# Kernel tuning notes

Measured on AMD Instinct MI355X. Metric: run time of the kernel, lower is better.

Reference implementation:

```python
import jax, jax.numpy as jnp
import numpy as np
from jax.ops import segment_sum

N_NODES = 50000
N_EDGES = 800000
IN_DIM, HID_DIM, OUT_DIM = 128, 128, 64
N_GRAPHS = 64


def setup_inputs() -> dict:
    key = jax.random.key(0)
    ks = jax.random.split(key, 8)
    x = jax.random.normal(ks[0], (N_NODES, IN_DIM), dtype=jnp.float32)
    edge_index = jax.random.randint(ks[1], (2, N_EDGES), 0, N_NODES, dtype=jnp.int64)
    batch = jnp.sort(jax.random.randint(ks[2], (N_NODES,), 0, N_GRAPHS, dtype=jnp.int64))
    # Glorot-ish init for GCNConv linear weights, zero bias (PyG default)
    W1 = jax.random.normal(ks[3], (IN_DIM, HID_DIM), dtype=jnp.float32) / np.sqrt(IN_DIM)
    b1 = jnp.zeros((HID_DIM,), dtype=jnp.float32)
    W2 = jax.random.normal(ks[4], (HID_DIM, OUT_DIM), dtype=jnp.float32) / np.sqrt(HID_DIM)
    b2 = jnp.zeros((OUT_DIM,), dtype=jnp.float32)
    return {"x": x, "W1": W1, "b1": b1, "W2": W2, "b2": b2,
            "edge_index": edge_index, "batch": batch, "num_graphs": N_GRAPHS}


def _gcn_conv(h, W, b, src, dst, deg_inv_sqrt, n_nodes):
    # h: [N, Fin] -> [N, Fout]; GCNConv: D^{-1/2}(A+I)D^{-1/2} (h W) + b
    hw = h @ W                                   # [N, Fout]
    norm = deg_inv_sqrt[src] * deg_inv_sqrt[dst] # [E]
    msg = hw[src] * norm[:, None]                # [E, Fout] (gather)
    agg = segment_sum(msg, dst, num_segments=n_nodes)  # scatter-add
    # self-loop contribution: norm_ii = deg_inv_sqrt[i]^2
    agg = agg + hw * (deg_inv_sqrt * deg_inv_sqrt)[:, None]
    return agg + b


def reference(x, W1, b1, W2, b2, edge_index, batch, num_graphs):
    n_nodes = x.shape[0]
    src, dst = edge_index[0], edge_index[1]
    # degree of A + I (self-loops added, as in PyG GCNConv default)
    deg = segment_sum(jnp.ones_like(dst, dtype=x.dtype), dst,
                      num_segments=n_nodes) + 1.0
    deg_inv_sqrt = jax.lax.rsqrt(deg)

    h = jax.nn.relu(_gcn_conv(x, W1, b1, src, dst, deg_inv_sqrt, n_nodes))
    h = jax.nn.relu(_gcn_conv(h, W2, b2, src, dst, deg_inv_sqrt, n_nodes))

    # global_mean_pool over batch ids
    sums = segment_sum(h, batch, num_segments=num_graphs)          # [G, Fout]
    counts = segment_sum(jnp.ones((n_nodes,), dtype=h.dtype), batch,
                         num_segments=num_graphs)                  # [G]
    return sums / jnp.maximum(counts, 1.0)[:, None]
```

## Files before the change

### kernel.cpp

```cpp
#include <hip/hip_runtime.h>

typedef float f4 __attribute__((ext_vector_type(4)));
typedef float f2 __attribute__((ext_vector_type(2)));
typedef short s8 __attribute__((ext_vector_type(8)));

union FU { unsigned u[4]; s8 s; };

__device__ __forceinline__ unsigned cvtpk(float lo, float hi){
  unsigned r;
  asm("v_cvt_pk_bf16_f32 %0, %1, %2" : "=v"(r) : "v"(lo), "v"(hi));
  return r;
}

__device__ __forceinline__ float bflo(unsigned v){ return __uint_as_float(v << 16); }
__device__ __forceinline__ float bfhi(unsigned v){ return __uint_as_float(v & 0xFFFF0000u); }

__device__ __forceinline__ int ld_idx(const void* p, int i, int is64){
  if (is64) return (int)((const long long*)p)[i];
  return ((const int*)p)[i];
}

__device__ __forceinline__ int detect64(const unsigned* __restrict__ e_raw, int e){
  int lane = threadIdx.x & 63;
  int lim = (e < 1024) ? e : 1024;
  int nz = 0;
  for (int i = lane; i < lim; i += 64) nz |= (e_raw[2*i + 1] != 0u);
  return (__ballot(nz != 0) == 0ull) ? 1 : 0;
}

template<int NC>
__device__ __forceinline__ void gemm_body(const float* __restrict__ X,
                                          const float* __restrict__ W,
                                          unsigned short* __restrict__ Yb,
                                          int n, int blk, char* Alds){
  constexpr int NCF = NC/16;
  constexpr int WPC = 8/NCF;
  constexpr int RT  = 8/WPC;
  const int tid  = threadIdx.x;
  const int wave = tid >> 6, lane = tid & 63;
  const int rb = blk * 128;
  const f4* X4 = (const f4*)X;

  const int cbase = (wave % NCF) * 16;
  const int rt0   = (wave / NCF) * RT;
  const int col   = cbase + (lane & 15);
  const int kr0   = (lane >> 4) * 8;
  FU bu[4];
#pragma unroll
  for (int ks = 0; ks < 4; ++ks){
    float wv[8];
#pragma unroll
    for (int j = 0; j < 8; ++j) wv[j] = W[(size_t)(ks*32 + kr0 + j)*NC + col];
#pragma unroll
    for (int q = 0; q < 4; ++q) bu[ks].u[q] = cvtpk(wv[2*q], wv[2*q+1]);
  }

  for (int i = tid; i < 128*32; i += 512){
    int row = i >> 5, kq = i & 31;
    int rsrc = rb + row; if (rsrc >= n) rsrc = n - 1;
    f4 xv = X4[(size_t)rsrc*32 + kq];
    unsigned lo = cvtpk(xv[0], xv[1]), hi = cvtpk(xv[2], xv[3]);
    int byte = (row*256 + kq*8) ^ ((row & 7) << 4);
    *reinterpret_cast<uint2*>(Alds + byte) = make_uint2(lo, hi);
  }
  __syncthreads();

  f4 acc[RT];
#pragma unroll
  for (int rt = 0; rt < RT; ++rt) acc[rt] = 0.0f;

#pragma unroll
  for (int rt = 0; rt < RT; ++rt){
    const int arow = (rt0 + rt)*16 + (lane & 15);
#pragma unroll
    for (int ks = 0; ks < 4; ++ks){
      int kb = ks*32 + kr0;
      int byte = (arow*256 + kb*2) ^ ((arow & 7) << 4);
      s8 a = *reinterpret_cast<const s8*>(Alds + byte);
      acc[rt] = __builtin_amdgcn_mfma_f32_16x16x32_bf16(a, bu[ks].s, acc[rt], 0, 0, 0);
    }
  }

#pragma unroll
  for (int rt = 0; rt < RT; ++rt){
    int rowb = rb + (rt0 + rt)*16 + 4*(lane >> 4);
#pragma unroll
    for (int r = 0; r < 4; ++r){
      int row = rowb + r;
      if (row < n) Yb[(size_t)row*NC + col] = (unsigned short)cvtpk(acc[rt][r], acc[rt][r]);
    }
  }
}

template<int NC>
__global__ __launch_bounds__(512) void gemm_k(const float* __restrict__ X,
                                              const float* __restrict__ W,
                                              unsigned short* __restrict__ Yb, int n){
  __shared__ int4 AldsV[2048];
  gemm_body<NC>(X, W, Yb, n, blockIdx.x, (char*)AldsV);
}

__global__ __launch_bounds__(512) void fused1_k(const float* __restrict__ X,
                                                const float* __restrict__ W1,
                                                unsigned short* __restrict__ Yb,
                                                const void* __restrict__ eidx,
                                                const void* __restrict__ batchp,
                                                int* __restrict__ counts,
                                                int* __restrict__ batch32,
                                                int n, int e, int GB, int CB){
  __shared__ int4 AldsV[2048];
  __shared__ int hist[512];
  int blk = blockIdx.x;
  if (blk < GB){
    gemm_body<128>(X, W1, Yb, n, blk, (char*)AldsV);
    return;
  }
  blk -= GB;
  const int NBK = (n + 127) >> 7;
  for (int i = threadIdx.x; i < NBK; i += 512) hist[i] = 0;
  __syncthreads();
  int is64 = detect64((const unsigned*)eidx, e);
  int CHK = (e + CB - 1) / CB;
  int beg = blk*CHK, end = min(e, beg + CHK);
  for (int i = beg + (int)threadIdx.x; i < end; i += 512){
    int d = ld_idx(eidx, e + i, is64);
    atomicAdd(&hist[d >> 7], 1);
  }
  __syncthreads();
  for (int i = threadIdx.x; i < NBK; i += 512) counts[i*CB + blk] = hist[i];
  for (int i = blk*512 + (int)threadIdx.x; i < n; i += CB*512)
    batch32[i] = ld_idx(batchp, i, is64);
}

__global__ void scanA_k(const int* __restrict__ counts, int* __restrict__ base,
                        int* __restrict__ bsum, int L){
  __shared__ int sh[256];
  int tid = threadIdx.x;
  int i = blockIdx.x*256 + tid;
  int v = (i < L) ? counts[i] : 0;
  sh[tid] = v; __syncthreads();
  for (int off = 1; off < 256; off <<= 1){
    int t = (tid >= off) ? sh[tid - off] : 0;
    __syncthreads();
    sh[tid] += t;
    __syncthreads();
  }
  if (i < L) base[i] = sh[tid] - v;
  if (tid == 255) bsum[blockIdx.x] = sh[255];
}

__global__ __launch_bounds__(512) void scanB2_k(int* __restrict__ bsum, int nb,
                                                float* __restrict__ outsum,
                                                int totalOut){
  __shared__ int sh[512];
  int tid = threadIdx.x;
  int v = (tid < nb) ? bsum[tid] : 0;
  sh[tid] = v; __syncthreads();
  for (int off = 1; off < 512; off <<= 1){
    int t = (tid >= off) ? sh[tid - off] : 0;
    __syncthreads();
    sh[tid] += t;
    __syncthreads();
  }
  if (tid < nb) bsum[tid] = sh[tid] - v;
  for (int k = tid; k < totalOut; k += 512) outsum[k] = 0.0f;
}

__global__ void scanC_k(int* __restrict__ base, const int* __restrict__ bsum,
                        int* __restrict__ bb, int* __restrict__ rowptr,
                        int L, int CB, int NBK, int n, int e){
  int i = blockIdx.x*256 + threadIdx.x;
  if (i < L){
    int vfin = base[i] + bsum[i >> 8];
    base[i] = vfin;
    if ((i & (CB - 1)) == 0) bb[i / CB] = vfin;
  }
  if (i == 0){ bb[NBK] = e; rowptr[n] = e; }
}

__global__ __launch_bounds__(512) void scat_k(const void* __restrict__ eidx,
                                              const int* __restrict__ base,
                                              int* __restrict__ packed,
                                              int n, int e, int CB){
  __shared__ int cur[512];
  int blk = blockIdx.x, tid = threadIdx.x;
  const int NBK = (n + 127) >> 7;
  for (int i = tid; i < NBK; i += 512) cur[i] = base[i*CB + blk];
  __syncthreads();
  int is64 = detect64((const unsigned*)eidx, e);
  int CHK = (e + CB - 1) / CB;
  int beg = blk*CHK, end = min(e, beg + CHK);
  for (int i = beg + tid; i < end; i += 512){
    int s = ld_idx(eidx, i, is64);
    int d = ld_idx(eidx, e + i, is64);
    int pos = atomicAdd(&cur[d >> 7], 1);
    packed[pos] = s | ((d & 127) << 16);
  }
}

#define CSR_CAP 6144
__global__ __launch_bounds__(256) void csr_k(const int* __restrict__ packed,
                                             const int* __restrict__ bb,
                                             int* __restrict__ esrcS,
                                             int* __restrict__ rowptr,
                                             float* __restrict__ dinv, int n){
  __shared__ int vals[CSR_CAP];
  __shared__ int hist[128], off[128], cur[128];
  int b = blockIdx.x, tid = threadIdx.x;
  int sbeg = bb[b], send = bb[b + 1];
  int m = send - sbeg;
  int mL = min(m, CSR_CAP);
  for (int i = tid; i < mL; i += 256) vals[i] = packed[sbeg + i];
  if (tid < 128) hist[tid] = 0;
  __syncthreads();
  for (int i = tid; i < m; i += 256){
    int v = (i < CSR_CAP) ? vals[i] : packed[sbeg + i];
    atomicAdd(&hist[(v >> 16) & 127], 1);
  }
  __syncthreads();
  if (tid < 128) off[tid] = hist[tid];
  __syncthreads();
  for (int o = 1; o < 128; o <<= 1){
    int v = 0;
    if (tid < 128 && tid >= o) v = off[tid - o];
    __syncthreads();
    if (tid < 128) off[tid] += v;
    __syncthreads();
  }
  if (tid < 128){
    int ex = off[tid] - hist[tid];
    cur[tid] = ex;
    int node = b*128 + tid;
    if (node < n){
      rowptr[node] = sbeg + ex;
      dinv[node] = rsqrtf((float)hist[tid] + 1.0f);
    }
  }
  __syncthreads();
  for (int i = tid; i < m; i += 256){
    int v = (i < CSR_CAP) ? vals[i] : packed[sbeg + i];
    int pos = atomicAdd(&cur[(v >> 16) & 127], 1);
    esrcS[sbeg + pos] = v & 0xFFFF;
  }
}

template<int NC>
__global__ __launch_bounds__(256) void agg_k(const unsigned short* __restrict__ HWb,
                                             const float* __restrict__ dinv,
                                             const int* __restrict__ rowptr,
                                             const int* __restrict__ esrcS,
                                             const float* __restrict__ bias,
                                             float* __restrict__ Hout, int n){
  int wid  = (blockIdx.x*256 + threadIdx.x) >> 6;
  int lane = threadIdx.x & 63;
  if (wid >= n) return;
  wid = __builtin_amdgcn_readfirstlane(wid);
  float di = dinv[wid];
  float di2 = di * di;
  int beg = __builtin_amdgcn_readfirstlane(rowptr[wid]);
  int end = __builtin_amdgcn_readfirstlane(rowptr[wid + 1]);
  if (NC == 128){
    unsigned sv = ((const unsigned*)(HWb + (size_t)wid*128))[lane];
    f2 acc;
    acc[0] = bflo(sv) * di2;
    acc[1] = bfhi(sv) * di2;
    int j = beg;
    for (; j + 8 <= end; j += 8){
      int s[8]; float dv[8]; unsigned v[8];
#pragma unroll
      for (int t = 0; t < 8; ++t) s[t] = esrcS[j + t];
#pragma unroll
      for (int t = 0; t < 8; ++t){
        dv[t] = dinv[s[t]];
        v[t] = ((const unsigned*)(HWb + (size_t)s[t]*128))[lane];
      }
#pragma unroll
      for (int t = 0; t < 8; ++t){
        float wt = dv[t] * di;
        acc[0] += bflo(v[t]) * wt;
        acc[1] += bfhi(v[t]) * wt;
      }
    }
    if (j + 4 <= end){
      int s[4]; float dv[4]; unsigned v[4];
#pragma unroll
      for (int t = 0; t < 4; ++t) s[t] = esrcS[j + t];
#pragma unroll
      for (int t = 0; t < 4; ++t){
        dv[t] = dinv[s[t]];
        v[t] = ((const unsigned*)(HWb + (size_t)s[t]*128))[lane];
      }
#pragma unroll
      for (int t = 0; t < 4; ++t){
        float wt = dv[t] * di;
        acc[0] += bflo(v[t]) * wt;
        acc[1] += bfhi(v[t]) * wt;
      }
      j += 4;
    }
    for (; j < end; ++j){
      int s = esrcS[j];
      float wt = dinv[s] * di;
      unsigned v = ((const unsigned*)(HWb + (size_t)s*128))[lane];
      acc[0] += bflo(v) * wt;
      acc[1] += bfhi(v) * wt;
    }
    f2 bb2 = ((const f2*)bias)[lane];
    acc += bb2;
    acc[0] = fmaxf(acc[0], 0.0f);
    acc[1] = fmaxf(acc[1], 0.0f);
    ((f2*)Hout)[(size_t)wid*64 + lane] = acc;
  } else {
    float acc = bflo((unsigned)HWb[(size_t)wid*64 + lane]) * di2;
    int j = beg;
    for (; j + 8 <= end; j += 8){
      int s[8]; float dv[8]; unsigned v[8];
#pragma unroll
      for (int t = 0; t < 8; ++t) s[t] = esrcS[j + t];
#pragma unroll
      for (int t = 0; t < 8; ++t){
        dv[t] = dinv[s[t]];
        v[t] = (unsigned)HWb[(size_t)s[t]*64 + lane];
      }
#pragma unroll
      for (int t = 0; t < 8; ++t) acc += bflo(v[t]) * (dv[t] * di);
    }
    if (j + 4 <= end){
      int s[4]; float dv[4]; unsigned v[4];
#pragma unroll
      for (int t = 0; t < 4; ++t) s[t] = esrcS[j + t];
#pragma unroll
      for (int t = 0; t < 4; ++t){
        dv[t] = dinv[s[t]];
        v[t] = (unsigned)HWb[(size_t)s[t]*64 + lane];
      }
#pragma unroll
      for (int t = 0; t < 4; ++t) acc += bflo(v[t]) * (dv[t] * di);
      j += 4;
    }
    for (; j < end; ++j){
      int s = esrcS[j];
      acc += bflo((unsigned)HWb[(size_t)s*64 + lane]) * (dinv[s] * di);
    }
    acc = fmaxf(acc + bias[lane], 0.0f);
    Hout[(size_t)wid*64 + lane] = acc;
  }
}

__global__ __launch_bounds__(256) void pool_k(const float* __restrict__ H2,
                                              const int* __restrict__ batch32,
                                              float* __restrict__ outsum, int n){
  int wid  = (blockIdx.x*256 + threadIdx.x) >> 6;
  int lane = threadIdx.x & 63;
  int start = wid * 8;
  if (start >= n) return;
  int cnt = min(8, n - start);
  float v[8]; int b[8];
#pragma unroll
  for (int t = 0; t < 8; ++t){
    int i = start + t; if (i >= n) i = n - 1;
    v[t] = H2[(size_t)i*64 + lane];
    b[t] = batch32[i];
  }
  float acc = 0.0f;
  int gcur = b[0];
#pragma unroll
  for (int t = 0; t < 8; ++t){
    if (t < cnt){
      if (b[t] != gcur){
        unsafeAtomicAdd(&outsum[gcur*64 + lane], acc);
        acc = 0.0f; gcur = b[t];
      }
      acc += v[t];
    }
  }
  unsafeAtomicAdd(&outsum[gcur*64 + lane], acc);
}

__global__ void fin_k(const float* __restrict__ outsum,
                      const int* __restrict__ batch32,
                      float* __restrict__ out, int n, int g){
  __shared__ int starts[257];
  int t = threadIdx.x;
  if (t <= g){
    int lo = 0, hi = n;
    while (lo < hi){ int mid = (lo + hi) >> 1; if (batch32[mid] < t) lo = mid + 1; else hi = mid; }
    starts[t] = lo;
  }
  __syncthreads();
  for (int idx = t; idx < (g << 6); idx += 256){
    int gi = idx >> 6;
    float c = (float)(starts[gi + 1] - starts[gi]);
    out[idx] = outsum[idx] / fmaxf(c, 1.0f);
  }
}

extern "C" void kernel_launch(void* const* d_in, const int* in_sizes, int n_in,
                              void* d_out, int out_size, void* d_ws, size_t ws_size,
                              hipStream_t stream){
  const float* x    = (const float*)d_in[0];
  const float* W1   = (const float*)d_in[1];
  const float* b1   = (const float*)d_in[2];
  const float* W2   = (const float*)d_in[3];
  const float* b2   = (const float*)d_in[4];
  const void*  eidx = d_in[5];
  const void*  batchp = d_in[6];
  const int n = in_sizes[0] / 128;
  const int e = in_sizes[5] / 2;
  const int g = out_size / 64;
  float* out = (float*)d_out;

  const int NBK = (n + 127) >> 7;
  const int CB  = 256;
  const int GB  = (n + 127) / 128;
  const int L   = NBK * CB;

  char* w = (char*)d_ws;
  int* counts  = (int*)w;
  int* base    = counts + (size_t)L;
  int* bsum    = base + (size_t)L;
  int  nb2     = (L + 255) / 256;
  int* bb      = bsum + nb2;
  int* rowptr  = bb + (NBK + 1);
  int* batch32 = rowptr + (n + 1);
  float* dinv  = (float*)(batch32 + n);
  float* outsum = dinv + n;
  int* packed  = (int*)(outsum + out_size);
  int* esrcS   = packed + e;
  size_t ofs = (size_t)((char*)(esrcS + e) - w);
  ofs = (ofs + 255) & ~(size_t)255;
  unsigned short* HWb = (unsigned short*)(w + ofs);
  size_t ofs2 = ofs + (size_t)n * 128 * 2;
  ofs2 = (ofs2 + 255) & ~(size_t)255;
  float* H = (float*)(w + ofs2);

  fused1_k<<<GB + CB, 512, 0, stream>>>(x, W1, HWb, eidx, batchp,
                                        counts, batch32, n, e, GB, CB);
  scanA_k<<<nb2, 256, 0, stream>>>(counts, base, bsum, L);
  scanB2_k<<<1, 512, 0, stream>>>(bsum, nb2, outsum, out_size);
  scanC_k<<<nb2, 256, 0, stream>>>(base, bsum, bb, rowptr, L, CB, NBK, n, e);
  scat_k<<<CB, 512, 0, stream>>>(eidx, base, packed, n, e, CB);
  csr_k<<<NBK, 256, 0, stream>>>(packed, bb, esrcS, rowptr, dinv, n);

  agg_k<128><<<(n + 3)/4, 256, 0, stream>>>(HWb, dinv, rowptr, esrcS, b1, H, n);
  gemm_k<64><<<GB, 512, 0, stream>>>(H, W2, HWb, n);
  agg_k<64><<<(n + 3)/4, 256, 0, stream>>>(HWb, dinv, rowptr, esrcS, b2, H, n);

  int pw = (n + 7)/8;
  pool_k<<<(pw + 3)/4, 256, 0, stream>>>(H, batch32, outsum, n);
  fin_k<<<1, 256, 0, stream>>>(outsum, batch32, out, n, g);
}
```

Measured before the change: 128.7 us.

## Store layer-1 output in bf16, drop scanC kernel, unroll aggregation by 16

The first aggregation now writes its ReLU output as packed bf16, and the second GEMM reads it directly without fp32 conversion. This halves the bytes of the intermediate H written and read. The scanC pass is removed: since CB equals the scan block size, bsum entries act as bucket bases and scat/csr add them in, which saves one kernel launch and one pass over base. The aggregation gather loops are widened from 8 to 16 edges per batch, trading registers for more loads in flight.

Result: faster. 124.1 us (-3.6%).

```diff
diff --git a/kernel.cpp b/kernel.cpp
--- a/kernel.cpp
+++ b/kernel.cpp
@@ -28,8 +28,8 @@
   return (__ballot(nz != 0) == 0ull) ? 1 : 0;
 }
 
-template<int NC>
-__device__ __forceinline__ void gemm_body(const float* __restrict__ X,
+template<int NC, int BIN>
+__device__ __forceinline__ void gemm_body(const void* __restrict__ Xv,
                                           const float* __restrict__ W,
                                           unsigned short* __restrict__ Yb,
                                           int n, int blk, char* Alds){
@@ -39,7 +39,6 @@
   const int tid  = threadIdx.x;
   const int wave = tid >> 6, lane = tid & 63;
   const int rb = blk * 128;
-  const f4* X4 = (const f4*)X;
 
   const int cbase = (wave % NCF) * 16;
   const int rt0   = (wave / NCF) * RT;
@@ -58,10 +57,15 @@
   for (int i = tid; i < 128*32; i += 512){
     int row = i >> 5, kq = i & 31;
     int rsrc = rb + row; if (rsrc >= n) rsrc = n - 1;
-    f4 xv = X4[(size_t)rsrc*32 + kq];
-    unsigned lo = cvtpk(xv[0], xv[1]), hi = cvtpk(xv[2], xv[3]);
+    uint2 dw;
+    if (BIN){
+      dw = ((const uint2*)Xv)[(size_t)rsrc*32 + kq];
+    } else {
+      f4 xv = ((const f4*)Xv)[(size_t)rsrc*32 + kq];
+      dw = make_uint2(cvtpk(xv[0], xv[1]), cvtpk(xv[2], xv[3]));
+    }
     int byte = (row*256 + kq*8) ^ ((row & 7) << 4);
-    *reinterpret_cast<uint2*>(Alds + byte) = make_uint2(lo, hi);
+    *reinterpret_cast<uint2*>(Alds + byte) = dw;
   }
   __syncthreads();
 
@@ -92,12 +96,12 @@
   }
 }
 
-template<int NC>
-__global__ __launch_bounds__(512) void gemm_k(const float* __restrict__ X,
+template<int NC, int BIN>
+__global__ __launch_bounds__(512) void gemm_k(const void* __restrict__ X,
                                               const float* __restrict__ W,
                                               unsigned short* __restrict__ Yb, int n){
   __shared__ int4 AldsV[2048];
-  gemm_body<NC>(X, W, Yb, n, blockIdx.x, (char*)AldsV);
+  gemm_body<NC, BIN>(X, W, Yb, n, blockIdx.x, (char*)AldsV);
 }
 
 __global__ __launch_bounds__(512) void fused1_k(const float* __restrict__ X,
@@ -112,7 +116,7 @@
   __shared__ int hist[512];
   int blk = blockIdx.x;
   if (blk < GB){
-    gemm_body<128>(X, W1, Yb, n, blk, (char*)AldsV);
+    gemm_body<128, 0>(X, W1, Yb, n, blk, (char*)AldsV);
     return;
   }
   blk -= GB;
@@ -150,8 +154,9 @@
 }
 
 __global__ __launch_bounds__(512) void scanB2_k(int* __restrict__ bsum, int nb,
+                                                int* __restrict__ rowptr,
                                                 float* __restrict__ outsum,
-                                                int totalOut){
+                                                int totalOut, int n, int e){
   __shared__ int sh[512];
   int tid = threadIdx.x;
   int v = (tid < nb) ? bsum[tid] : 0;
@@ -163,29 +168,20 @@
     __syncthreads();
   }
   if (tid < nb) bsum[tid] = sh[tid] - v;
+  if (tid == nb - 1) bsum[nb] = sh[tid];
+  if (tid == 0) rowptr[n] = e;
   for (int k = tid; k < totalOut; k += 512) outsum[k] = 0.0f;
-}
-
-__global__ void scanC_k(int* __restrict__ base, const int* __restrict__ bsum,
-                        int* __restrict__ bb, int* __restrict__ rowptr,
-                        int L, int CB, int NBK, int n, int e){
-  int i = blockIdx.x*256 + threadIdx.x;
-  if (i < L){
-    int vfin = base[i] + bsum[i >> 8];
-    base[i] = vfin;
-    if ((i & (CB - 1)) == 0) bb[i / CB] = vfin;
-  }
-  if (i == 0){ bb[NBK] = e; rowptr[n] = e; }
 }
 
 __global__ __launch_bounds__(512) void scat_k(const void* __restrict__ eidx,
                                               const int* __restrict__ base,
+                                              const int* __restrict__ bsum,
                                               int* __restrict__ packed,
                                               int n, int e, int CB){
   __shared__ int cur[512];
   int blk = blockIdx.x, tid = threadIdx.x;
   const int NBK = (n + 127) >> 7;
-  for (int i = tid; i < NBK; i += 512) cur[i] = base[i*CB + blk];
+  for (int i = tid; i < NBK; i += 512) cur[i] = bsum[i] + base[i*CB + blk];
   __syncthreads();
   int is64 = detect64((const unsigned*)eidx, e);
   int CHK = (e + CB - 1) / CB;
@@ -200,14 +196,14 @@
 
 #define CSR_CAP 6144
 __global__ __launch_bounds__(256) void csr_k(const int* __restrict__ packed,
-                                             const int* __restrict__ bb,
+                                             const int* __restrict__ bsum,
                                              int* __restrict__ esrcS,
                                              int* __restrict__ rowptr,
                                              float* __restrict__ dinv, int n){
   __shared__ int vals[CSR_CAP];
   __shared__ int hist[128], off[128], cur[128];
   int b = blockIdx.x, tid = threadIdx.x;
-  int sbeg = bb[b], send = bb[b + 1];
+  int sbeg = bsum[b], send = bsum[b + 1];
   int m = send - sbeg;
   int mL = min(m, CSR_CAP);
   for (int i = tid; i < mL; i += 256) vals[i] = packed[sbeg + i];
@@ -244,13 +240,13 @@
   }
 }
 
-template<int NC>
+template<int NC, int OB>
 __global__ __launch_bounds__(256) void agg_k(const unsigned short* __restrict__ HWb,
                                              const float* __restrict__ dinv,
                                              const int* __restrict__ rowptr,
                                              const int* __restrict__ esrcS,
                                              const float* __restrict__ bias,
-                                             float* __restrict__ Hout, int n){
+                                             void* __restrict__ Hout, int n){
   int wid  = (blockIdx.x*256 + threadIdx.x) >> 6;
   int lane = threadIdx.x & 63;
   if (wid >= n) return;
@@ -261,27 +257,25 @@
   int end = __builtin_amdgcn_readfirstlane(rowptr[wid + 1]);
   if (NC == 128){
     unsigned sv = ((const unsigned*)(HWb + (size_t)wid*128))[lane];
-    f2 acc;
-    acc[0] = bflo(sv) * di2;
-    acc[1] = bfhi(sv) * di2;
+    float a0 = bflo(sv) * di2, a1 = bfhi(sv) * di2;
     int j = beg;
-    for (; j + 8 <= end; j += 8){
-      int s[8]; float dv[8]; unsigned v[8];
-#pragma unroll
-      for (int t = 0; t < 8; ++t) s[t] = esrcS[j + t];
-#pragma unroll
-      for (int t = 0; t < 8; ++t){
+    for (; j + 16 <= end; j += 16){
+      int s[16]; float dv[16]; unsigned v[16];
+#pragma unroll
+      for (int t = 0; t < 16; ++t) s[t] = esrcS[j + t];
+#pragma unroll
+      for (int t = 0; t < 16; ++t){
         dv[t] = dinv[s[t]];
         v[t] = ((const unsigned*)(HWb + (size_t)s[t]*128))[lane];
       }
 #pragma unroll
-      for (int t = 0; t < 8; ++t){
+      for (int t = 0; t < 16; ++t){
         float wt = dv[t] * di;
-        acc[0] += bflo(v[t]) * wt;
-        acc[1] += bfhi(v[t]) * wt;
-      }
-    }
-    if (j + 4 <= end){
+        a0 += bflo(v[t]) * wt;
+        a1 += bfhi(v[t]) * wt;
+      }
+    }
+    for (; j + 4 <= end; j += 4){
       int s[4]; float dv[4]; unsigned v[4];
 #pragma unroll
       for (int t = 0; t < 4; ++t) s[t] = esrcS[j + t];
@@ -293,39 +287,42 @@
 #pragma unroll
       for (int t = 0; t < 4; ++t){
         float wt = dv[t] * di;
-        acc[0] += bflo(v[t]) * wt;
-        acc[1] += bfhi(v[t]) * wt;
-      }
-      j += 4;
+        a0 += bflo(v[t]) * wt;
+        a1 += bfhi(v[t]) * wt;
+      }
     }
     for (; j < end; ++j){
       int s = esrcS[j];
       float wt = dinv[s] * di;
       unsigned v = ((const unsigned*)(HWb + (size_t)s*128))[lane];
-      acc[0] += bflo(v) * wt;
-      acc[1] += bfhi(v) * wt;
-    }
-    f2 bb2 = ((const f2*)bias)[lane];
-    acc += bb2;
-    acc[0] = fmaxf(acc[0], 0.0f);
-    acc[1] = fmaxf(acc[1], 0.0f);
-    ((f2*)Hout)[(size_t)wid*64 + lane] = acc;
+      a0 += bflo(v) * wt;
+      a1 += bfhi(v) * wt;
+    }
+    f2 bb = ((const f2*)bias)[lane];
+    a0 = fmaxf(a0 + bb[0], 0.0f);
+    a1 = fmaxf(a1 + bb[1], 0.0f);
+    if (OB){
+      ((unsigned*)Hout)[(size_t)wid*64 + lane] = cvtpk(a0, a1);
+    } else {
+      f2 r; r[0] = a0; r[1] = a1;
+      ((f2*)Hout)[(size_t)wid*64 + lane] = r;
+    }
   } else {
     float acc = bflo((unsigned)HWb[(size_t)wid*64 + lane]) * di2;
     int j = beg;
-    for (; j + 8 <= end; j += 8){
-      int s[8]; float dv[8]; unsigned v[8];
-#pragma unroll
-      for (int t = 0; t < 8; ++t) s[t] = esrcS[j + t];
-#pragma unroll
-      for (int t = 0; t < 8; ++t){
+    for (; j + 16 <= end; j += 16){
+      int s[16]; float dv[16]; unsigned v[16];
+#pragma unroll
+      for (int t = 0; t < 16; ++t) s[t] = esrcS[j + t];
+#pragma unroll
+      for (int t = 0; t < 16; ++t){
         dv[t] = dinv[s[t]];
         v[t] = (unsigned)HWb[(size_t)s[t]*64 + lane];
       }
 #pragma unroll
-      for (int t = 0; t < 8; ++t) acc += bflo(v[t]) * (dv[t] * di);
-    }
-    if (j + 4 <= end){
+      for (int t = 0; t < 16; ++t) acc += bflo(v[t]) * (dv[t] * di);
+    }
+    for (; j + 4 <= end; j += 4){
       int s[4]; float dv[4]; unsigned v[4];
 #pragma unroll
       for (int t = 0; t < 4; ++t) s[t] = esrcS[j + t];
@@ -336,14 +333,13 @@
       }
 #pragma unroll
       for (int t = 0; t < 4; ++t) acc += bflo(v[t]) * (dv[t] * di);
-      j += 4;
     }
     for (; j < end; ++j){
       int s = esrcS[j];
       acc += bflo((unsigned)HWb[(size_t)s*64 + lane]) * (dinv[s] * di);
     }
     acc = fmaxf(acc + bias[lane], 0.0f);
-    Hout[(size_t)wid*64 + lane] = acc;
+    ((float*)Hout)[(size_t)wid*64 + lane] = acc;
   }
 }
 
@@ -419,9 +415,7 @@
   int* counts  = (int*)w;
   int* base    = counts + (size_t)L;
   int* bsum    = base + (size_t)L;
-  int  nb2     = (L + 255) / 256;
-  int* bb      = bsum + nb2;
-  int* rowptr  = bb + (NBK + 1);
+  int* rowptr  = bsum + (NBK + 1);
   int* batch32 = rowptr + (n + 1);
   float* dinv  = (float*)(batch32 + n);
   float* outsum = dinv + n;
@@ -432,21 +426,23 @@
   unsigned short* HWb = (unsigned short*)(w + ofs);
   size_t ofs2 = ofs + (size_t)n * 128 * 2;
   ofs2 = (ofs2 + 255) & ~(size_t)255;
-  float* H = (float*)(w + ofs2);
+  unsigned short* Hb = (unsigned short*)(w + ofs2);
+  size_t ofs3 = ofs2 + (size_t)n * 128 * 2;
+  ofs3 = (ofs3 + 255) & ~(size_t)255;
+  float* H2 = (float*)(w + ofs3);
 
   fused1_k<<<GB + CB, 512, 0, stream>>>(x, W1, HWb, eidx, batchp,
                                         counts, batch32, n, e, GB, CB);
-  scanA_k<<<nb2, 256, 0, stream>>>(counts, base, bsum, L);
-  scanB2_k<<<1, 512, 0, stream>>>(bsum, nb2, outsum, out_size);
-  scanC_k<<<nb2, 256, 0, stream>>>(base, bsum, bb, rowptr, L, CB, NBK, n, e);
-  scat_k<<<CB, 512, 0, stream>>>(eidx, base, packed, n, e, CB);
-  csr_k<<<NBK, 256, 0, stream>>>(packed, bb, esrcS, rowptr, dinv, n);
-
-  agg_k<128><<<(n + 3)/4, 256, 0, stream>>>(HWb, dinv, rowptr, esrcS, b1, H, n);
-  gemm_k<64><<<GB, 512, 0, stream>>>(H, W2, HWb, n);
-  agg_k<64><<<(n + 3)/4, 256, 0, stream>>>(HWb, dinv, rowptr, esrcS, b2, H, n);
+  scanA_k<<<NBK, 256, 0, stream>>>(counts, base, bsum, L);
+  scanB2_k<<<1, 512, 0, stream>>>(bsum, NBK, rowptr, outsum, out_size, n, e);
+  scat_k<<<CB, 512, 0, stream>>>(eidx, base, bsum, packed, n, e, CB);
+  csr_k<<<NBK, 256, 0, stream>>>(packed, bsum, esrcS, rowptr, dinv, n);
+
+  agg_k<128, 1><<<(n + 3)/4, 256, 0, stream>>>(HWb, dinv, rowptr, esrcS, b1, Hb, n);
+  gemm_k<64, 1><<<GB, 512, 0, stream>>>(Hb, W2, HWb, n);
+  agg_k<64, 0><<<(n + 3)/4, 256, 0, stream>>>(HWb, dinv, rowptr, esrcS, b2, H2, n);
 
   int pw = (n + 7)/8;
-  pool_k<<<(pw + 3)/4, 256, 0, stream>>>(H, batch32, outsum, n);
+  pool_k<<<(pw + 3)/4, 256, 0, stream>>>(H2, batch32, outsum, n);
   fin_k<<<1, 256, 0, stream>>>(outsum, batch32, out, n, g);
 }
```
